# Performance work log

Measured on AMD Instinct MI355X. Metric: run time of the kernel, lower is better.

The kernel has to match this reference:

```python
import jax, jax.numpy as jnp
import numpy as np

V, E, H, S, B = 32000, 256, 256, 128, 64
HID = 30  # DENSE_MLP_HIDDEN_SIZE


def setup_inputs() -> dict:
    key = jax.random.key(0)
    ks = jax.random.split(key, 12)
    concepts = jax.random.randint(ks[0], (S, B), 0, V)
    concepts_lengths = jax.random.randint(ks[1], (B,), 1, S + 1).at[0].set(S)
    sE = 1.0 / np.sqrt(E)
    sH = 1.0 / np.sqrt(H)
    s2H = 1.0 / np.sqrt(2 * H)
    sHID = 1.0 / np.sqrt(HID)
    return {
        "concepts": concepts,
        "concepts_lengths": concepts_lengths,
        "embedding": jax.random.normal(ks[2], (V, E), jnp.float32) * 0.02,
        "Wih_f": jax.random.normal(ks[3], (4 * H, E), jnp.float32) * sE,
        "Whh_f": jax.random.normal(ks[4], (4 * H, H), jnp.float32) * sH,
        "b_f": jax.random.normal(ks[5], (4 * H,), jnp.float32) * sH,
        "Wih_b": jax.random.normal(ks[6], (4 * H, E), jnp.float32) * sE,
        "Whh_b": jax.random.normal(ks[7], (4 * H, H), jnp.float32) * sH,
        "b_b": jax.random.normal(ks[8], (4 * H,), jnp.float32) * sH,
        "Ua": jax.random.normal(ks[9], (HID, 2 * H), jnp.float32) * s2H,
        "Wa": jax.random.normal(ks[10], (HID, 2 * H), jnp.float32) * s2H,
        "va": jax.random.normal(ks[11], (1, HID), jnp.float32) * sHID,
    }


def _lstm(x, Wih, Whh, b):
    # x: (S, B, E) -> outputs (S, B, H). PyTorch gate order: i, f, g, o.
    Bsz = x.shape[1]
    Hd = Whh.shape[1]
    h0 = jnp.zeros((Bsz, Hd), x.dtype)
    c0 = jnp.zeros((Bsz, Hd), x.dtype)

    def step(carry, xt):
        h, c = carry
        gates = xt @ Wih.T + h @ Whh.T + b
        i, f, g, o = jnp.split(gates, 4, axis=-1)
        c = jax.nn.sigmoid(f) * c + jax.nn.sigmoid(i) * jnp.tanh(g)
        h = jax.nn.sigmoid(o) * jnp.tanh(c)
        return (h, c), h

    _, hs = jax.lax.scan(step, (h0, c0), x)
    return hs


def _encode(concepts, concepts_lengths, embedding, Wih_f, Whh_f, b_f, Wih_b, Whh_b, b_b):
    emb = embedding[concepts]  # (S, B, E)
    t = jnp.arange(S)[:, None]  # (S, 1)
    lens = concepts_lengths[None, :]  # (1, B)
    valid = t < lens  # (S, B)
    # reverse each sequence within its valid length (packed biLSTM semantics)
    rev_idx = jnp.where(valid, lens - 1 - t, t)  # (S, B)
    fwd = _lstm(emb, Wih_f, Whh_f, b_f)
    x_rev = jnp.take_along_axis(emb, rev_idx[:, :, None], axis=0)
    bwd_rev = _lstm(x_rev, Wih_b, Whh_b, b_b)
    bwd = jnp.take_along_axis(bwd_rev, rev_idx[:, :, None], axis=0)
    h = jnp.concatenate([fwd, bwd], axis=-1) * valid[:, :, None]  # zero padding like pad_packed
    return h.transpose(1, 0, 2)  # (B, S, 2H)


def _edge_scores(enc, Ua, Wa, va):
    # scores[b, i, j] = va @ tanh(Ua @ enc[b,i] + Wa @ enc[b,j])
    u = enc @ Ua.T  # (B, S, HID) parent term
    w = enc @ Wa.T  # (B, S, HID) child term
    return jnp.tanh(u[:, :, None, :] + w[:, None, :, :]) @ va[0]  # (B, S, S)


def reference(concepts, concepts_lengths, embedding, Wih_f, Whh_f, b_f,
              Wih_b, Whh_b, b_b, Ua, Wa, va):
    enc = _encode(concepts, concepts_lengths, embedding,
                  Wih_f, Whh_f, b_f, Wih_b, Whh_b, b_b)
    scores = _edge_scores(enc, Ua, Wa, va)
    predictions = jnp.where(jax.nn.sigmoid(scores) >= 0.5, 1, 0)
    return scores, predictions
```

## Files before the change

### kernel.cpp

```cpp
#include <hip/hip_runtime.h>

#define V_  32000
#define E_  256
#define H_  256
#define S_  128
#define B_  64
#define HID_ 30

typedef float f32x2 __attribute__((ext_vector_type(2)));

__device__ __forceinline__ float sigmoid_fast(float x) {
    return __builtin_amdgcn_rcpf(1.f + __expf(-x));
}
__device__ __forceinline__ float fast_tanh(float x) {
    return 1.f - 2.f * __builtin_amdgcn_rcpf(1.f + __expf(2.f * x));
}
__device__ __forceinline__ float sigmoid_acc(float x) {
    return 1.0f / (1.0f + expf(-x));
}

__device__ __forceinline__ void store_l2x2(unsigned long long* p,
                                           unsigned long long a,
                                           unsigned long long b) {
    asm volatile("global_store_dwordx2 %2, %0, off\n\t"
                 "global_store_dwordx2 %2, %1, off offset:8"
                 :: "v"(a), "v"(b), "v"(p) : "memory");
}
__device__ __forceinline__ void load_l2x2(const unsigned long long* p,
                                          unsigned long long& a,
                                          unsigned long long& b) {
    asm volatile("global_load_dwordx2 %0, %2, off sc0\n\t"
                 "global_load_dwordx2 %1, %2, off offset:8 sc0\n\t"
                 "s_waitcnt vmcnt(0)"
                 : "=&v"(a), "=&v"(b) : "v"(p) : "memory");
}

__device__ __forceinline__ void barrier_lds() {
    asm volatile("s_waitcnt lgkmcnt(0)" ::: "memory");
    __builtin_amdgcn_s_barrier();
    __builtin_amdgcn_sched_barrier(0);
}

__global__ __launch_bounds__(256) void prep_stream_kernel(
    const float* __restrict__ Whh_f, const float* __restrict__ Whh_b,
    float4* __restrict__ sT, unsigned long long* __restrict__ Fch) {
    int i = blockIdx.x * 256 + threadIdx.x;
    if (i < 16 * 1024) {
        int r = i & 1023;
        int q = i >> 10;
        int j = q & 3;
        int side = (q >> 2) & 1;
        int dir = q >> 3;
        const float* Whh = dir ? Whh_b : Whh_f;
        const float* src = Whh + (size_t)r * H_ + side * 128 + 112 + 4 * j;
        sT[(size_t)q * 1024 + r] = make_float4(src[0], src[1], src[2], src[3]);
    }
    for (size_t k = i; k < 524288; k += 16384) Fch[k] = 0ull;
}

#define GKC 32
#define GLD 132

__global__ __launch_bounds__(256, 4) void gemm2_kernel(
    const int* __restrict__ concepts, const float* __restrict__ embedding,
    const float* __restrict__ Wih_f, const float* __restrict__ Wih_b,
    float* __restrict__ Xg) {
    __shared__ float As[GKC][GLD];
    __shared__ float Bs[GKC][GLD];
    const int dir = blockIdx.y;
    const float* Wih = dir ? Wih_b : Wih_f;
    const int mt = blockIdx.x >> 3;
    const int nt = blockIdx.x & 7;
    const int m0 = mt * 128, n0 = nt * 128;
    const int t = threadIdx.x;
    const int tm = (t & 15) * 4;
    const int tn = (t >> 4) * 4;

    int cid[4], rr[4];
#pragma unroll
    for (int i = 0; i < 4; ++i) {
        int flat = t + 256 * i;
        rr[i] = flat >> 3;
        cid[i] = concepts[m0 + rr[i]];
    }

    f32x2 acc2[8][4];
#pragma unroll
    for (int i = 0; i < 8; ++i)
#pragma unroll
        for (int j = 0; j < 4; ++j) acc2[i][j] = (f32x2){0.f, 0.f};

    for (int kk = 0; kk < E_; kk += GKC) {
        __syncthreads();
#pragma unroll
        for (int i = 0; i < 4; ++i) {
            int flat = t + 256 * i;
            int r = rr[i];
            int kq = (flat & 7) * 4;
            float4 av = *(const float4*)&embedding[(size_t)cid[i] * E_ + kk + kq];
            float4 bv = *(const float4*)&Wih[(size_t)(n0 + r) * E_ + kk + kq];
            As[kq + 0][r] = av.x; As[kq + 1][r] = av.y;
            As[kq + 2][r] = av.z; As[kq + 3][r] = av.w;
            Bs[kq + 0][r] = bv.x; Bs[kq + 1][r] = bv.y;
            Bs[kq + 2][r] = bv.z; Bs[kq + 3][r] = bv.w;
        }
        __syncthreads();
#pragma unroll
        for (int k = 0; k < GKC; ++k) {
            float4 a0 = *(const float4*)&As[k][tm];
            float4 a1 = *(const float4*)&As[k][tm + 64];
            float4 b0 = *(const float4*)&Bs[k][tn];
            float4 b1 = *(const float4*)&Bs[k][tn + 64];
            float am[8] = {a0.x, a0.y, a0.z, a0.w, a1.x, a1.y, a1.z, a1.w};
            f32x2 bn2[4] = {(f32x2){b0.x, b0.y}, (f32x2){b0.z, b0.w},
                            (f32x2){b1.x, b1.y}, (f32x2){b1.z, b1.w}};
#pragma unroll
            for (int i = 0; i < 8; ++i) {
                f32x2 ai = (f32x2){am[i], am[i]};
#pragma unroll
                for (int j = 0; j < 4; ++j)
                    acc2[i][j] = __builtin_elementwise_fma(ai, bn2[j], acc2[i][j]);
            }
        }
    }
    float* out = Xg + ((size_t)dir * 8192 + m0) * 1024 + n0;
#pragma unroll
    for (int i = 0; i < 8; ++i) {
        int mr = (i < 4) ? (tm + i) : (tm + 60 + i);
        *(float4*)&out[(size_t)mr * 1024 + tn] =
            make_float4(acc2[i][0].x, acc2[i][0].y, acc2[i][1].x, acc2[i][1].y);
        *(float4*)&out[(size_t)mr * 1024 + tn + 64] =
            make_float4(acc2[i][2].x, acc2[i][2].y, acc2[i][3].x, acc2[i][3].y);
    }
}

#define RP_  38
#define LPD_ 18

__global__ __launch_bounds__(512)
__attribute__((amdgpu_waves_per_eu(2, 2)))
void lstm_ks3_kernel(
    const float* __restrict__ Xg,
    const float* __restrict__ Whh_f, const float* __restrict__ Whh_b,
    const float* __restrict__ b_f, const float* __restrict__ b_b,
    const int* __restrict__ lens,
    float* __restrict__ enc,
    unsigned long long* __restrict__ Fch,
    unsigned long long* __restrict__ Sch,
    const float4* __restrict__ sT) {
    extern __shared__ float4 Wl4[];
    __shared__ float h_sh[2][128];
    const int w = blockIdx.x;
    const int side = w >> 7;
    const int P = w & 127;
    const int dir = P & 1, b = P >> 1;
    const int t = threadIdx.x;
    const int wav = t >> 6;
    const int lane = t & 63;
    const int li = lane & 31;
    const int half = lane >> 5;
    const int qw = (wav & 1) | ((wav >> 2) << 1);
    const bool mine = (((wav >> 1) & 1) == side);
    const int hs = mine ? side : (side ^ 1);
    const int hcol = (hs << 7) + (qw << 5) + li;
    const int rA = hcol + half * 256;
    const int rB = hcol + 512 + half * 256;
    const int base = side << 7;
    const int idx = (qw << 6) + lane;
    const float* Whh = dir ? Whh_b : Whh_f;
    const int len = lens[b];

    f32x2 w0[RP_], w1[RP_];
    {
        const f32x2* p0 = (const f32x2*)(Whh + (size_t)rA * H_ + base);
        const f32x2* p1 = (const f32x2*)(Whh + (size_t)rB * H_ + base);
#pragma unroll
        for (int j = 0; j < RP_; ++j) { w0[j] = p0[j]; w1[j] = p1[j]; }
#pragma unroll
        for (int j = 0; j < LPD_; ++j) {
            f32x2 a = p0[RP_ + j], c2 = p1[RP_ + j];
            Wl4[j * 512 + t] = make_float4(a.x, a.y, c2.x, c2.y);
        }
    }
    const f32x2* sT2 = (const f32x2*)(sT + (size_t)(dir * 8 + side * 4) * 1024);
    f32x2 s0[8], s1[8];
#pragma unroll
    for (int k = 0; k < 4; ++k) {
        s0[2 * k]     = sT2[2 * (k * 1024 + rA)];
        s0[2 * k + 1] = sT2[2 * (k * 1024 + rA) + 1];
        s1[2 * k]     = sT2[2 * (k * 1024 + rB)];
        s1[2 * k + 1] = sT2[2 * (k * 1024 + rB) + 1];
    }
#pragma unroll
    for (int j = 0; j < RP_; ++j) {
        asm volatile("" : "+v"(w0[j]), "+v"(w1[j]));
    }
#pragma unroll
    for (int k = 0; k < 8; ++k) {
        asm volatile("" : "+v"(s0[k]), "+v"(s1[k]));
    }
    const float* bias = dir ? b_b : b_f;
    const float bias0 = bias[rA], bias1 = bias[rB];

    unsigned long long* fwb = Fch + (((size_t)P * 2 + 0) * 2 + side) * 512 + 2 * idx;
    const unsigned long long* frb =
        Fch + (((size_t)P * 2 + 0) * 2 + (side ^ 1)) * 512 + 2 * idx;
    unsigned long long* swb = Sch + (((size_t)P * 2 + 0) * 2 + side) * 512 + 2 * idx;
    const unsigned long long* srb =
        Sch + (((size_t)P * 2 + 0) * 2 + (side ^ 1)) * 512 + 2 * idx;

    if (t < 128) h_sh[0][t] = 0.f;
    float c = 0.f;
    __syncthreads();

    int srow = dir ? (len - 1) : 0;
    float x0 = 0.f, x1 = 0.f;
    if (mine) {
        const float* xp = Xg + ((size_t)dir * 8192 + (size_t)srow * B_ + b) * 1024;
        x0 = xp[rA]; x1 = xp[rB];
    }

    for (int s = 0; s < S_; ++s) {
        int srow_n = 0;
        float x0n = 0.f, x1n = 0.f;
        if (s + 1 < S_) {
            int ns = s + 1;
            srow_n = dir ? ((ns < len) ? (len - 1 - ns) : ns) : ns;
            if (mine) {
                const float* xp =
                    Xg + ((size_t)dir * 8192 + (size_t)srow_n * B_ + b) * 1024;
                x0n = xp[rA]; x1n = xp[rB];
            }
        }

        const float4* hb4 = (const float4*)h_sh[s & 1];
        f32x2 a0 = (f32x2){0.f, 0.f}, a1 = (f32x2){0.f, 0.f};
#pragma unroll
        for (int q = 0; q < 19; ++q) {
            float4 hq = hb4[q];
            f32x2 hA = (f32x2){hq.x, hq.y}, hB = (f32x2){hq.z, hq.w};
            a0 = __builtin_elementwise_fma(w0[2 * q], hA, a0);
            a0 = __builtin_elementwise_fma(w0[2 * q + 1], hB, a0);
            a1 = __builtin_elementwise_fma(w1[2 * q], hA, a1);
            a1 = __builtin_elementwise_fma(w1[2 * q + 1], hB, a1);
        }
#pragma unroll
        for (int jj = 0; jj < 9; ++jj) {
            float4 hq = hb4[19 + jj];
            f32x2 hA = (f32x2){hq.x, hq.y}, hB = (f32x2){hq.z, hq.w};
            float4 wE = Wl4[(2 * jj) * 512 + t];
            float4 wO = Wl4[(2 * jj + 1) * 512 + t];
            a0 = __builtin_elementwise_fma((f32x2){wE.x, wE.y}, hA, a0);
            a1 = __builtin_elementwise_fma((f32x2){wE.z, wE.w}, hA, a1);
            a0 = __builtin_elementwise_fma((f32x2){wO.x, wO.y}, hB, a0);
            a1 = __builtin_elementwise_fma((f32x2){wO.z, wO.w}, hB, a1);
        }
#pragma unroll
        for (int k = 0; k < 4; ++k) {
            float4 hq = hb4[28 + k];
            f32x2 hA = (f32x2){hq.x, hq.y}, hB = (f32x2){hq.z, hq.w};
            a0 = __builtin_elementwise_fma(s0[2 * k], hA, a0);
            a0 = __builtin_elementwise_fma(s0[2 * k + 1], hB, a0);
            a1 = __builtin_elementwise_fma(s1[2 * k], hA, a1);
            a1 = __builtin_elementwise_fma(s1[2 * k + 1], hB, a1);
        }
        float p0 = a0.x + a0.y, p1 = a1.x + a1.y;

        const unsigned tag = (unsigned)(s + 1);
        const size_t par = (size_t)(s & 1) << 10;
        if (!mine) {
            unsigned long long k0 =
                ((unsigned long long)tag << 32) | (unsigned long long)__float_as_uint(p0);
            unsigned long long k1 =
                ((unsigned long long)tag << 32) | (unsigned long long)__float_as_uint(p1);
            store_l2x2(fwb + par, k0, k1);
            unsigned long long* sb = swb + par;
            __hip_atomic_store(sb, k0, __ATOMIC_RELAXED, __HIP_MEMORY_SCOPE_AGENT);
            __hip_atomic_store(sb + 1, k1, __ATOMIC_RELAXED, __HIP_MEMORY_SCOPE_AGENT);
        } else {
            const unsigned long long* fr = frb + par;
            const unsigned long long* sr = srb + par;
            float q0f, q1f;
            for (;;) {
                unsigned long long f0, f1;
                load_l2x2(fr, f0, f1);
                if ((unsigned)(f0 >> 32) == tag && (unsigned)(f1 >> 32) == tag) {
                    q0f = __uint_as_float((unsigned)f0);
                    q1f = __uint_as_float((unsigned)f1);
                    break;
                }
                unsigned long long a0q = __hip_atomic_load(
                    sr, __ATOMIC_RELAXED, __HIP_MEMORY_SCOPE_AGENT);
                unsigned long long a1q = __hip_atomic_load(
                    sr + 1, __ATOMIC_RELAXED, __HIP_MEMORY_SCOPE_AGENT);
                if ((unsigned)(a0q >> 32) == tag && (unsigned)(a1q >> 32) == tag) {
                    q0f = __uint_as_float((unsigned)a0q);
                    q1f = __uint_as_float((unsigned)a1q);
                    break;
                }
            }
            float g0 = p0 + q0f + bias0 + x0;
            float g1 = p1 + q1f + bias1 + x1;
            float e0 = sigmoid_fast(g0);
            float u, v;
            if (half == 0) { u = e0 * fast_tanh(g1); v = 0.f; }
            else           { u = e0; v = sigmoid_fast(g1); }
            float fx = __shfl_xor(u, 32);
            float ox = __shfl_xor(v, 32);
            if (half == 0) {
                c = fx * c + u;
                float h = ox * fast_tanh(c);
                h_sh[(s + 1) & 1][(qw << 5) + li] = h;
                int orow = dir ? srow : s;
                enc[((size_t)b * S_ + orow) * 512 + dir * H_ + base + (qw << 5) + li] =
                    (orow < len) ? h : 0.f;
            }
        }
        barrier_lds();

        srow = srow_n;
        x0 = x0n; x1 = x1n;
    }
}

__global__ __launch_bounds__(256) void uw_kernel(
    const float* __restrict__ enc, const float* __restrict__ Ua,
    const float* __restrict__ Wa, float* __restrict__ U, float* __restrict__ Wout) {
    __shared__ float wgt[60][129];
    __shared__ float erow[4][128];
    const int tid = threadIdx.x;
    const int b = blockIdx.y, s0 = blockIdx.x * 16;
    const int rl = tid >> 6;
    const int d = tid & 63;
    const int dd = d & 31;
    const int isW = d >> 5;
    float acc[4];
#pragma unroll
    for (int i = 0; i < 4; ++i) acc[i] = 0.f;

    for (int kk = 0; kk < 4; ++kk) {
        __syncthreads();
        for (int i = tid; i < 30 * 128; i += 256) {
            int r = i >> 7, k = i & 127;
            wgt[r][k] = Ua[(size_t)r * 512 + kk * 128 + k];
            wgt[r + 30][k] = Wa[(size_t)r * 512 + kk * 128 + k];
        }
        for (int chunk = 0; chunk < 4; ++chunk) {
            __syncthreads();
            for (int i = tid; i < 4 * 128; i += 256) {
                int r = i >> 7, k = i & 127;
                erow[r][k] = enc[((size_t)b * S_ + (s0 + chunk * 4 + r)) * 512 + kk * 128 + k];
            }
            __syncthreads();
            if (dd < HID_) {
                const float* wr = wgt[dd + 30 * isW];
                const float* er = erow[rl];
                float a = acc[chunk];
#pragma unroll
                for (int k = 0; k < 128; ++k) a = fmaf(er[k], wr[k], a);
                acc[chunk] = a;
            }
        }
    }
    if (dd < HID_) {
        float* dst = isW ? Wout : U;
#pragma unroll
        for (int chunk = 0; chunk < 4; ++chunk)
            dst[((size_t)b * S_ + (s0 + chunk * 4 + rl)) * 32 + dd] = acc[chunk];
    }
}

__global__ __launch_bounds__(256) void scores_kernel(
    const float* __restrict__ U, const float* __restrict__ W,
    const float* __restrict__ va,
    float* __restrict__ scores, float* __restrict__ preds) {
    __shared__ float w_sh[128][31];
    const int b = blockIdx.y, i0 = blockIdx.x * 16;
    const int tid = threadIdx.x;

    float va_r[HID_];
#pragma unroll
    for (int d2 = 0; d2 < HID_; ++d2) va_r[d2] = va[d2];

    for (int i = tid; i < 128 * HID_; i += 256) {
        int r = i / HID_, d2 = i - r * HID_;
        w_sh[r][d2] = W[((size_t)b * S_ + r) * 32 + d2];
    }
    __syncthreads();

    const int il = tid >> 4;
    const int jb = (tid & 15) * 8;
    float u_r[HID_];
    const float* urow = U + ((size_t)b * S_ + i0 + il) * 32;
#pragma unroll
    for (int d2 = 0; d2 < HID_; ++d2) u_r[d2] = urow[d2];

    const size_t obase = ((size_t)b * S_ + (i0 + il)) * S_;
    for (int jj = 0; jj < 8; ++jj) {
        int j = jb + jj;
        float acc = 0.f;
#pragma unroll
        for (int d2 = 0; d2 < HID_; ++d2)
            acc = fmaf(va_r[d2], fast_tanh(u_r[d2] + w_sh[j][d2]), acc);
        scores[obase + j] = acc;
        preds[obase + j] = (sigmoid_acc(acc) >= 0.5f) ? 1.f : 0.f;
    }
}

extern "C" void kernel_launch(void* const* d_in, const int* in_sizes, int n_in,
                              void* d_out, int out_size, void* d_ws, size_t ws_size,
                              hipStream_t stream) {
    (void)in_sizes; (void)n_in; (void)out_size; (void)ws_size;
    const int* concepts = (const int*)d_in[0];
    const int* lens = (const int*)d_in[1];
    const float* embedding = (const float*)d_in[2];
    const float* Wih_f = (const float*)d_in[3];
    const float* Whh_f = (const float*)d_in[4];
    const float* b_f = (const float*)d_in[5];
    const float* Wih_b = (const float*)d_in[6];
    const float* Whh_b = (const float*)d_in[7];
    const float* b_b = (const float*)d_in[8];
    const float* Ua = (const float*)d_in[9];
    const float* Wa = (const float*)d_in[10];
    const float* va = (const float*)d_in[11];

    char* ws = (char*)d_ws;
    float* Xg = (float*)(ws + 0);
    float* enc = (float*)(ws + 67108864);
    float* U = (float*)(ws + 83886080);
    float* W = (float*)(ws + 84934656);
    unsigned long long* Fch = (unsigned long long*)(ws + 85983232);
    unsigned long long* Sch = (unsigned long long*)(ws + 88080384);
    float4* sT = (float4*)(ws + 90177536);

    float* scores = (float*)d_out;
    float* preds = scores + (size_t)B_ * S_ * S_;

    hipLaunchKernelGGL(prep_stream_kernel, dim3(64), dim3(256), 0, stream,
                       Whh_f, Whh_b, sT, Fch);
    hipLaunchKernelGGL(gemm2_kernel, dim3(512, 2), dim3(256), 0, stream,
                       concepts, embedding, Wih_f, Wih_b, Xg);

    {
        const float* XgA = Xg;
        void* ka[] = {(void*)&XgA, (void*)&Whh_f, (void*)&Whh_b, (void*)&b_f,
                      (void*)&b_b, (void*)&lens, (void*)&enc, (void*)&Fch,
                      (void*)&Sch, (void*)&sT};
        (void)hipLaunchCooperativeKernel((const void*)lstm_ks3_kernel, dim3(256),
                                         dim3(512), ka,
                                         LPD_ * 512 * sizeof(float4), stream);
    }

    hipLaunchKernelGGL(uw_kernel, dim3(8, 64), dim3(256), 0, stream,
                       enc, Ua, Wa, U, W);
    hipLaunchKernelGGL(scores_kernel, dim3(8, 64), dim3(256), 0, stream,
                       U, W, va, scores, preds);
}
```

Before: 531.3 us.

## Fuse weight prep and input-projection GEMM into cooperative LSTM kernel

Moves the Whh stream-layout prep, the flag-buffer zeroing and the embedding×Wih input GEMM into the front of the cooperative LSTM kernel, separated from the recurrence by a grid-wide sync. This removes two kernel launches and their gaps. The GEMM now runs on 256 blocks of 512 threads using the LSTM's dynamic shared memory, with 128×512 tiles and a larger per-thread accumulator. The risk is lower GEMM occupancy and throughput, higher register pressure in the fused kernel, and the cost of the grid sync.

```diff
diff --git a/kernel.cpp b/kernel.cpp
--- a/kernel.cpp
+++ b/kernel.cpp
@@ -1,4 +1,7 @@
 #include <hip/hip_runtime.h>
+#include <hip/hip_cooperative_groups.h>
+
+namespace cg = cooperative_groups;
 
 #define V_  32000
 #define E_  256
@@ -41,120 +44,128 @@
     __builtin_amdgcn_sched_barrier(0);
 }
 
-__global__ __launch_bounds__(256) void prep_stream_kernel(
-    const float* __restrict__ Whh_f, const float* __restrict__ Whh_b,
-    float4* __restrict__ sT, unsigned long long* __restrict__ Fch) {
-    int i = blockIdx.x * 256 + threadIdx.x;
-    if (i < 16 * 1024) {
-        int r = i & 1023;
-        int q = i >> 10;
-        int j = q & 3;
-        int side = (q >> 2) & 1;
-        int dir = q >> 3;
-        const float* Whh = dir ? Whh_b : Whh_f;
-        const float* src = Whh + (size_t)r * H_ + side * 128 + 112 + 4 * j;
-        sT[(size_t)q * 1024 + r] = make_float4(src[0], src[1], src[2], src[3]);
-    }
-    for (size_t k = i; k < 524288; k += 16384) Fch[k] = 0ull;
-}
-
-#define GKC 32
-#define GLD 132
-
-__global__ __launch_bounds__(256, 4) void gemm2_kernel(
-    const int* __restrict__ concepts, const float* __restrict__ embedding,
-    const float* __restrict__ Wih_f, const float* __restrict__ Wih_b,
-    float* __restrict__ Xg) {
-    __shared__ float As[GKC][GLD];
-    __shared__ float Bs[GKC][GLD];
-    const int dir = blockIdx.y;
-    const float* Wih = dir ? Wih_b : Wih_f;
-    const int mt = blockIdx.x >> 3;
-    const int nt = blockIdx.x & 7;
-    const int m0 = mt * 128, n0 = nt * 128;
-    const int t = threadIdx.x;
-    const int tm = (t & 15) * 4;
-    const int tn = (t >> 4) * 4;
-
-    int cid[4], rr[4];
-#pragma unroll
-    for (int i = 0; i < 4; ++i) {
-        int flat = t + 256 * i;
-        rr[i] = flat >> 3;
-        cid[i] = concepts[m0 + rr[i]];
-    }
-
-    f32x2 acc2[8][4];
-#pragma unroll
-    for (int i = 0; i < 8; ++i)
-#pragma unroll
-        for (int j = 0; j < 4; ++j) acc2[i][j] = (f32x2){0.f, 0.f};
-
-    for (int kk = 0; kk < E_; kk += GKC) {
-        __syncthreads();
-#pragma unroll
-        for (int i = 0; i < 4; ++i) {
-            int flat = t + 256 * i;
-            int r = rr[i];
-            int kq = (flat & 7) * 4;
-            float4 av = *(const float4*)&embedding[(size_t)cid[i] * E_ + kk + kq];
-            float4 bv = *(const float4*)&Wih[(size_t)(n0 + r) * E_ + kk + kq];
-            As[kq + 0][r] = av.x; As[kq + 1][r] = av.y;
-            As[kq + 2][r] = av.z; As[kq + 3][r] = av.w;
-            Bs[kq + 0][r] = bv.x; Bs[kq + 1][r] = bv.y;
-            Bs[kq + 2][r] = bv.z; Bs[kq + 3][r] = bv.w;
-        }
-        __syncthreads();
-#pragma unroll
-        for (int k = 0; k < GKC; ++k) {
-            float4 a0 = *(const float4*)&As[k][tm];
-            float4 a1 = *(const float4*)&As[k][tm + 64];
-            float4 b0 = *(const float4*)&Bs[k][tn];
-            float4 b1 = *(const float4*)&Bs[k][tn + 64];
-            float am[8] = {a0.x, a0.y, a0.z, a0.w, a1.x, a1.y, a1.z, a1.w};
-            f32x2 bn2[4] = {(f32x2){b0.x, b0.y}, (f32x2){b0.z, b0.w},
-                            (f32x2){b1.x, b1.y}, (f32x2){b1.z, b1.w}};
-#pragma unroll
-            for (int i = 0; i < 8; ++i) {
-                f32x2 ai = (f32x2){am[i], am[i]};
-#pragma unroll
-                for (int j = 0; j < 4; ++j)
-                    acc2[i][j] = __builtin_elementwise_fma(ai, bn2[j], acc2[i][j]);
-            }
-        }
-    }
-    float* out = Xg + ((size_t)dir * 8192 + m0) * 1024 + n0;
-#pragma unroll
-    for (int i = 0; i < 8; ++i) {
-        int mr = (i < 4) ? (tm + i) : (tm + 60 + i);
-        *(float4*)&out[(size_t)mr * 1024 + tn] =
-            make_float4(acc2[i][0].x, acc2[i][0].y, acc2[i][1].x, acc2[i][1].y);
-        *(float4*)&out[(size_t)mr * 1024 + tn + 64] =
-            make_float4(acc2[i][2].x, acc2[i][2].y, acc2[i][3].x, acc2[i][3].y);
-    }
-}
-
 #define RP_  38
 #define LPD_ 18
 
 __global__ __launch_bounds__(512)
 __attribute__((amdgpu_waves_per_eu(2, 2)))
-void lstm_ks3_kernel(
-    const float* __restrict__ Xg,
+void lstm_fused_kernel(
+    const int* __restrict__ concepts,
+    const float* __restrict__ embedding,
+    const float* __restrict__ Wih_f, const float* __restrict__ Wih_b,
+    float* __restrict__ Xg,
     const float* __restrict__ Whh_f, const float* __restrict__ Whh_b,
     const float* __restrict__ b_f, const float* __restrict__ b_b,
     const int* __restrict__ lens,
     float* __restrict__ enc,
     unsigned long long* __restrict__ Fch,
     unsigned long long* __restrict__ Sch,
-    const float4* __restrict__ sT) {
+    float4* __restrict__ sT) {
     extern __shared__ float4 Wl4[];
     __shared__ float h_sh[2][128];
     const int w = blockIdx.x;
+    const int t = threadIdx.x;
+
+    if (t < 64) {
+        int i = (w << 6) + t;
+        int r = i & 1023;
+        int q = i >> 10;
+        int jq = q & 3;
+        int sideq = (q >> 2) & 1;
+        int dirq = q >> 3;
+        const float* WhhQ = dirq ? Whh_b : Whh_f;
+        const float* src = WhhQ + (size_t)r * H_ + sideq * 128 + 112 + 4 * jq;
+        sT[(size_t)q * 1024 + r] = make_float4(src[0], src[1], src[2], src[3]);
+    }
+#pragma unroll
+    for (int i = 0; i < 4; ++i)
+        Fch[(size_t)w * 2048 + t + 512 * i] = 0ull;
+
+    {
+        const int rowblk = w >> 1;
+        const int chg = w & 1;
+        const int dirg = rowblk >> 6;
+        const int m0 = (rowblk & 63) * 128;
+        const int n0 = chg * 512;
+        const float* WihG = dirg ? Wih_b : Wih_f;
+        float* As_ = (float*)Wl4;
+        float* Bs_ = As_ + 32 * 132;
+
+        int cidg[2];
+#pragma unroll
+        for (int i = 0; i < 2; ++i) {
+            int flat = t + 512 * i;
+            cidg[i] = concepts[m0 + (flat >> 3)];
+        }
+        const int tmg = (t & 15) * 4;
+        const int tng = (t >> 4) * 16;
+
+        f32x2 accg[8][8];
+#pragma unroll
+        for (int i = 0; i < 8; ++i)
+#pragma unroll
+            for (int j = 0; j < 8; ++j) accg[i][j] = (f32x2){0.f, 0.f};
+
+        for (int kk = 0; kk < E_; kk += 32) {
+            __syncthreads();
+#pragma unroll
+            for (int i = 0; i < 2; ++i) {
+                int flat = t + 512 * i;
+                int r = flat >> 3;
+                int kq = (flat & 7) * 4;
+                float4 av = *(const float4*)&embedding[(size_t)cidg[i] * E_ + kk + kq];
+                As_[(kq + 0) * 132 + r] = av.x; As_[(kq + 1) * 132 + r] = av.y;
+                As_[(kq + 2) * 132 + r] = av.z; As_[(kq + 3) * 132 + r] = av.w;
+            }
+#pragma unroll
+            for (int i = 0; i < 8; ++i) {
+                int flat = t + 512 * i;
+                int r = flat >> 3;
+                int kq = (flat & 7) * 4;
+                float4 bv = *(const float4*)&WihG[(size_t)(n0 + r) * E_ + kk + kq];
+                Bs_[(kq + 0) * 516 + r] = bv.x; Bs_[(kq + 1) * 516 + r] = bv.y;
+                Bs_[(kq + 2) * 516 + r] = bv.z; Bs_[(kq + 3) * 516 + r] = bv.w;
+            }
+            __syncthreads();
+#pragma unroll
+            for (int k = 0; k < 32; ++k) {
+                float4 a0 = *(const float4*)&As_[k * 132 + tmg];
+                float4 a1 = *(const float4*)&As_[k * 132 + tmg + 64];
+                float am[8] = {a0.x, a0.y, a0.z, a0.w, a1.x, a1.y, a1.z, a1.w};
+                float4 b0 = *(const float4*)&Bs_[k * 516 + tng];
+                float4 b1 = *(const float4*)&Bs_[k * 516 + tng + 4];
+                float4 b2 = *(const float4*)&Bs_[k * 516 + tng + 8];
+                float4 b3 = *(const float4*)&Bs_[k * 516 + tng + 12];
+                f32x2 bn2[8] = {(f32x2){b0.x, b0.y}, (f32x2){b0.z, b0.w},
+                                (f32x2){b1.x, b1.y}, (f32x2){b1.z, b1.w},
+                                (f32x2){b2.x, b2.y}, (f32x2){b2.z, b2.w},
+                                (f32x2){b3.x, b3.y}, (f32x2){b3.z, b3.w}};
+#pragma unroll
+                for (int i = 0; i < 8; ++i) {
+                    f32x2 ai = (f32x2){am[i], am[i]};
+#pragma unroll
+                    for (int j = 0; j < 8; ++j)
+                        accg[i][j] = __builtin_elementwise_fma(ai, bn2[j], accg[i][j]);
+                }
+            }
+        }
+        float* outg = Xg + ((size_t)dirg * 8192 + m0) * 1024 + n0;
+#pragma unroll
+        for (int i = 0; i < 8; ++i) {
+            int mr = (i < 4) ? (tmg + i) : (tmg + 60 + i);
+#pragma unroll
+            for (int j2 = 0; j2 < 4; ++j2)
+                *(float4*)&outg[(size_t)mr * 1024 + tng + 4 * j2] =
+                    make_float4(accg[i][2 * j2].x, accg[i][2 * j2].y,
+                                accg[i][2 * j2 + 1].x, accg[i][2 * j2 + 1].y);
+        }
+    }
+
+    cg::this_grid().sync();
+
     const int side = w >> 7;
     const int P = w & 127;
     const int dir = P & 1, b = P >> 1;
-    const int t = threadIdx.x;
     const int wav = t >> 6;
     const int lane = t & 63;
     const int li = lane & 31;
@@ -436,18 +447,13 @@
     float* scores = (float*)d_out;
     float* preds = scores + (size_t)B_ * S_ * S_;
 
-    hipLaunchKernelGGL(prep_stream_kernel, dim3(64), dim3(256), 0, stream,
-                       Whh_f, Whh_b, sT, Fch);
-    hipLaunchKernelGGL(gemm2_kernel, dim3(512, 2), dim3(256), 0, stream,
-                       concepts, embedding, Wih_f, Wih_b, Xg);
-
     {
-        const float* XgA = Xg;
-        void* ka[] = {(void*)&XgA, (void*)&Whh_f, (void*)&Whh_b, (void*)&b_f,
-                      (void*)&b_b, (void*)&lens, (void*)&enc, (void*)&Fch,
-                      (void*)&Sch, (void*)&sT};
-        (void)hipLaunchCooperativeKernel((const void*)lstm_ks3_kernel, dim3(256),
-                                         dim3(512), ka,
+        void* ka[] = {(void*)&concepts, (void*)&embedding, (void*)&Wih_f,
+                      (void*)&Wih_b, (void*)&Xg, (void*)&Whh_f, (void*)&Whh_b,
+                      (void*)&b_f, (void*)&b_b, (void*)&lens, (void*)&enc,
+                      (void*)&Fch, (void*)&Sch, (void*)&sT};
+        (void)hipLaunchCooperativeKernel((const void*)lstm_fused_kernel,
+                                         dim3(256), dim3(512), ka,
                                          LPD_ * 512 * sizeof(float4), stream);
     }
 
```

New measurement: 574.3 us. 8.1% more time.

## Convert embedding and Wih to fp16 and compute input GEMM with MFMA

Applied to the files above, without the earlier changes.

The prep kernel now converts the full embedding table and both Wih matrices to fp16 in workspace. The input-projection GEMM is rewritten to use 16x16x32 f16 MFMA instructions, loading operands directly from global memory instead of staging them through LDS. The aim is to replace scalar fp32 FMA throughput with matrix-core throughput, at the cost of fp16 input precision and an extra pass that converts the whole 32000x256 table on every call.

```diff
diff --git a/kernel.cpp b/kernel.cpp
--- a/kernel.cpp
+++ b/kernel.cpp
@@ -8,6 +8,9 @@
 #define HID_ 30
 
 typedef float f32x2 __attribute__((ext_vector_type(2)));
+typedef float f32x4v __attribute__((ext_vector_type(4)));
+typedef _Float16 f16x4 __attribute__((ext_vector_type(4)));
+typedef _Float16 f16x8 __attribute__((ext_vector_type(8)));
 
 __device__ __forceinline__ float sigmoid_fast(float x) {
     return __builtin_amdgcn_rcpf(1.f + __expf(-x));
@@ -43,95 +46,89 @@
 
 __global__ __launch_bounds__(256) void prep_stream_kernel(
     const float* __restrict__ Whh_f, const float* __restrict__ Whh_b,
-    float4* __restrict__ sT, unsigned long long* __restrict__ Fch) {
-    int i = blockIdx.x * 256 + threadIdx.x;
-    if (i < 16 * 1024) {
-        int r = i & 1023;
-        int q = i >> 10;
-        int j = q & 3;
+    const float* __restrict__ embedding,
+    const float* __restrict__ Wih_f, const float* __restrict__ Wih_b,
+    float4* __restrict__ sT, unsigned long long* __restrict__ Fch,
+    _Float16* __restrict__ embF16, _Float16* __restrict__ WihF16) {
+    const int gtid = blockIdx.x * 256 + threadIdx.x;
+    if (gtid < 16 * 1024) {
+        int r = gtid & 1023;
+        int q = gtid >> 10;
+        int jq = q & 3;
         int side = (q >> 2) & 1;
         int dir = q >> 3;
         const float* Whh = dir ? Whh_b : Whh_f;
-        const float* src = Whh + (size_t)r * H_ + side * 128 + 112 + 4 * j;
+        const float* src = Whh + (size_t)r * H_ + side * 128 + 112 + 4 * jq;
         sT[(size_t)q * 1024 + r] = make_float4(src[0], src[1], src[2], src[3]);
     }
-    for (size_t k = i; k < 524288; k += 16384) Fch[k] = 0ull;
-}
-
-#define GKC 32
-#define GLD 132
+#pragma unroll
+    for (int i = 0; i < 8; ++i) Fch[(size_t)gtid + 65536 * i] = 0ull;
+
+    const float4* e4 = (const float4*)embedding;
+    for (int k4 = gtid; k4 < 2048000; k4 += 65536) {
+        float4 v = e4[k4];
+        *(f16x4*)(embF16 + 4 * (size_t)k4) =
+            (f16x4){(_Float16)v.x, (_Float16)v.y, (_Float16)v.z, (_Float16)v.w};
+    }
+    {
+        float4 v = ((const float4*)Wih_f)[gtid];
+        *(f16x4*)(WihF16 + 4 * (size_t)gtid) =
+            (f16x4){(_Float16)v.x, (_Float16)v.y, (_Float16)v.z, (_Float16)v.w};
+        float4 u = ((const float4*)Wih_b)[gtid];
+        *(f16x4*)(WihF16 + 262144 + 4 * (size_t)gtid) =
+            (f16x4){(_Float16)u.x, (_Float16)u.y, (_Float16)u.z, (_Float16)u.w};
+    }
+}
 
 __global__ __launch_bounds__(256, 4) void gemm2_kernel(
-    const int* __restrict__ concepts, const float* __restrict__ embedding,
-    const float* __restrict__ Wih_f, const float* __restrict__ Wih_b,
-    float* __restrict__ Xg) {
-    __shared__ float As[GKC][GLD];
-    __shared__ float Bs[GKC][GLD];
+    const int* __restrict__ concepts, const _Float16* __restrict__ embF16,
+    const _Float16* __restrict__ WihF16, float* __restrict__ Xg) {
     const int dir = blockIdx.y;
-    const float* Wih = dir ? Wih_b : Wih_f;
+    const _Float16* WihF = WihF16 + (size_t)dir * 262144;
     const int mt = blockIdx.x >> 3;
     const int nt = blockIdx.x & 7;
     const int m0 = mt * 128, n0 = nt * 128;
     const int t = threadIdx.x;
-    const int tm = (t & 15) * 4;
-    const int tn = (t >> 4) * 4;
-
-    int cid[4], rr[4];
-#pragma unroll
-    for (int i = 0; i < 4; ++i) {
-        int flat = t + 256 * i;
-        rr[i] = flat >> 3;
-        cid[i] = concepts[m0 + rr[i]];
-    }
-
-    f32x2 acc2[8][4];
-#pragma unroll
-    for (int i = 0; i < 8; ++i)
-#pragma unroll
-        for (int j = 0; j < 4; ++j) acc2[i][j] = (f32x2){0.f, 0.f};
-
-    for (int kk = 0; kk < E_; kk += GKC) {
-        __syncthreads();
-#pragma unroll
-        for (int i = 0; i < 4; ++i) {
-            int flat = t + 256 * i;
-            int r = rr[i];
-            int kq = (flat & 7) * 4;
-            float4 av = *(const float4*)&embedding[(size_t)cid[i] * E_ + kk + kq];
-            float4 bv = *(const float4*)&Wih[(size_t)(n0 + r) * E_ + kk + kq];
-            As[kq + 0][r] = av.x; As[kq + 1][r] = av.y;
-            As[kq + 2][r] = av.z; As[kq + 3][r] = av.w;
-            Bs[kq + 0][r] = bv.x; Bs[kq + 1][r] = bv.y;
-            Bs[kq + 2][r] = bv.z; Bs[kq + 3][r] = bv.w;
-        }
-        __syncthreads();
-#pragma unroll
-        for (int k = 0; k < GKC; ++k) {
-            float4 a0 = *(const float4*)&As[k][tm];
-            float4 a1 = *(const float4*)&As[k][tm + 64];
-            float4 b0 = *(const float4*)&Bs[k][tn];
-            float4 b1 = *(const float4*)&Bs[k][tn + 64];
-            float am[8] = {a0.x, a0.y, a0.z, a0.w, a1.x, a1.y, a1.z, a1.w};
-            f32x2 bn2[4] = {(f32x2){b0.x, b0.y}, (f32x2){b0.z, b0.w},
-                            (f32x2){b1.x, b1.y}, (f32x2){b1.z, b1.w}};
-#pragma unroll
-            for (int i = 0; i < 8; ++i) {
-                f32x2 ai = (f32x2){am[i], am[i]};
-#pragma unroll
-                for (int j = 0; j < 4; ++j)
-                    acc2[i][j] = __builtin_elementwise_fma(ai, bn2[j], acc2[i][j]);
-            }
-        }
-    }
-    float* out = Xg + ((size_t)dir * 8192 + m0) * 1024 + n0;
-#pragma unroll
-    for (int i = 0; i < 8; ++i) {
-        int mr = (i < 4) ? (tm + i) : (tm + 60 + i);
-        *(float4*)&out[(size_t)mr * 1024 + tn] =
-            make_float4(acc2[i][0].x, acc2[i][0].y, acc2[i][1].x, acc2[i][1].y);
-        *(float4*)&out[(size_t)mr * 1024 + tn + 64] =
-            make_float4(acc2[i][2].x, acc2[i][2].y, acc2[i][3].x, acc2[i][3].y);
-    }
+    const int v = t >> 6;
+    const int lane = t & 63;
+    const int lr = lane & 15;
+    const int kg = lane >> 4;
+    const int ko = kg * 8;
+
+    const int cid0 = concepts[m0 + 32 * v + lr];
+    const int cid1 = concepts[m0 + 32 * v + 16 + lr];
+    const _Float16* a0p = embF16 + (size_t)cid0 * 256 + ko;
+    const _Float16* a1p = embF16 + (size_t)cid1 * 256 + ko;
+    const _Float16* bp = WihF + (size_t)(n0 + lr) * 256 + ko;
+
+    f32x4v acc[2][8];
+#pragma unroll
+    for (int i = 0; i < 2; ++i)
+#pragma unroll
+        for (int j = 0; j < 8; ++j) acc[i][j] = (f32x4v){0.f, 0.f, 0.f, 0.f};
+
+#pragma unroll
+    for (int kk = 0; kk < 256; kk += 32) {
+        f16x8 af0 = *(const f16x8*)(a0p + kk);
+        f16x8 af1 = *(const f16x8*)(a1p + kk);
+#pragma unroll
+        for (int ct = 0; ct < 8; ++ct) {
+            f16x8 bf = *(const f16x8*)(bp + ct * 4096 + kk);
+            acc[0][ct] = __builtin_amdgcn_mfma_f32_16x16x32_f16(
+                af0, bf, acc[0][ct], 0, 0, 0);
+            acc[1][ct] = __builtin_amdgcn_mfma_f32_16x16x32_f16(
+                af1, bf, acc[1][ct], 0, 0, 0);
+        }
+    }
+    float* outp = Xg + ((size_t)dir * 8192 + m0 + 32 * v) * 1024 + n0 + lr;
+#pragma unroll
+    for (int rb = 0; rb < 2; ++rb)
+#pragma unroll
+        for (int ct = 0; ct < 8; ++ct)
+#pragma unroll
+            for (int r = 0; r < 4; ++r)
+                outp[(size_t)(16 * rb + kg * 4 + r) * 1024 + 16 * ct] =
+                    acc[rb][ct][r];
 }
 
 #define RP_  38
@@ -432,14 +429,17 @@
     unsigned long long* Fch = (unsigned long long*)(ws + 85983232);
     unsigned long long* Sch = (unsigned long long*)(ws + 88080384);
     float4* sT = (float4*)(ws + 90177536);
+    _Float16* embF16 = (_Float16*)(ws + 67108864);
+    _Float16* WihF16 = (_Float16*)(ws + 83886080);
 
     float* scores = (float*)d_out;
     float* preds = scores + (size_t)B_ * S_ * S_;
 
-    hipLaunchKernelGGL(prep_stream_kernel, dim3(64), dim3(256), 0, stream,
-                       Whh_f, Whh_b, sT, Fch);
+    hipLaunchKernelGGL(prep_stream_kernel, dim3(256), dim3(256), 0, stream,
+                       Whh_f, Whh_b, embedding, Wih_f, Wih_b, sT, Fch,
+                       embF16, WihF16);
     hipLaunchKernelGGL(gemm2_kernel, dim3(512, 2), dim3(256), 0, stream,
-                       concepts, embedding, Wih_f, Wih_b, Xg);
+                       concepts, embF16, WihF16, Xg);
 
     {
         const float* XgA = Xg;
```

Result: faster. 484.4 us (-8.8%).
